# Performance work log

Hardware: AMD Instinct MI355X
Metric: run time of the kernel (lower is better)

The kernel has to match this reference:

```python
import jax, jax.numpy as jnp
import numpy as np


def _pair_table(L):
    # 0,0 0,1 ... upper-triangular (start,end) enumeration, P = L*(L+1)/2
    starts = np.concatenate([np.arange(i + 1) for i in range(L)])
    ends = np.concatenate([np.full(i + 1, i) for i in range(L)])
    return starts.astype(np.int32), ends.astype(np.int32)


def setup_inputs() -> dict:
    key = jax.random.key(0)
    ks = jax.random.split(key, 10)
    B, L, Q, H, T = 8, 384, 64, 256, 9
    p = lambda k, shape: jax.random.normal(k, shape, jnp.float32) * 0.02
    return dict(
        batch_hiddens=jax.random.normal(ks[0], (B, L, H), jnp.float32),
        batch_masks=jnp.ones((B, L), dtype=bool),
        queries=jax.random.normal(ks[1], (B, Q, H), jnp.float32),
        queries_locs=jax.random.uniform(ks[2], (B, Q, 2), jnp.float32) * L,
        queries_logits=jax.random.normal(ks[3], (B, Q, T + 1), jnp.float32),
        Wc=p(ks[4], (H, T + 1)), bc=jnp.zeros((T + 1,), jnp.float32),
        Wq=p(ks[5], (H, 2 * H)), bq=jnp.zeros((2 * H,), jnp.float32),
        Wv=p(ks[6], (H, 2 * H)), bv=jnp.zeros((2 * H,), jnp.float32),
        Wo=p(ks[7], (H, 2)), bo=jnp.zeros((2,), jnp.float32),
        Wf=p(ks[8], (H, 2)), bf=jnp.zeros((2,), jnp.float32),
    )


def reference(batch_hiddens, batch_masks, queries, queries_locs, queries_logits,
              Wc, bc, Wq, bq, Wv, bv, Wo, bo, Wf, bf):
    B, L, H = batch_hiddens.shape
    Q = queries.shape[1]
    starts, ends = _pair_table(L)  # static: L known at trace time

    # label probabilities: softmax(prior logits + classifier(queries))
    labels_pros = jax.nn.softmax(queries_logits + queries @ Wc + bc, axis=-1)

    # biaffine start/end channels
    qh = (queries @ Wq + bq).reshape(B, Q, 2, H)        # [B,Q,2,H]
    ch = (batch_hiddens @ Wv + bv).reshape(B, L, 2, H)  # [B,L,2,H]
    score = jnp.einsum('bqch,bvch->bcqv', qh, ch) / jnp.sqrt(jnp.float32(H))
    score = jnp.where(batch_masks[:, None, None, :], score, -1e8)

    # span score via start/end table gather: [B,Q,P]
    span = score[:, 0][:, :, starts] + score[:, 1][:, :, ends]
    mask_p = batch_masks[:, ends]  # [B,P] valid if end token valid

    # locator: gaussian distribution over spans centered at refined locations
    offset = queries @ Wo + bo                      # [B,Q,2]
    factors = jax.nn.softplus(queries @ Wf + bf)    # [B,Q,2] positive widths
    locs = queries_locs + offset                    # [B,Q,2]
    pairs_f = jnp.stack([jnp.asarray(starts), jnp.asarray(ends)], axis=-1).astype(jnp.float32)  # [P,2]
    d2 = (pairs_f[None, None] - locs[:, :, None]) ** 2          # [B,Q,P,2]
    weight = jnp.exp(-(d2 * factors[:, :, None]).sum(-1))       # [B,Q,P]
    weight = jnp.where(mask_p[:, None, :], weight, 0.0)

    # weighted softmax over spans
    m = jnp.max(span, axis=-1, keepdims=True)
    e = jnp.exp(span - m) * weight
    locs_pros = e / (jnp.sum(e, axis=-1, keepdims=True) + 1e-12)
    return labels_pros, locs_pros
```

## Files before the change

### kernel.cpp

```cpp
#include <hip/hip_runtime.h>
#include <math.h>

#define B_    8
#define L_    384
#define Q_    64
#define H_    256
#define R_    512
#define P_    73920
#define NF4   18480
#define QF4   4620

#define WS_WVT   0
#define WS_HIDT  131072
#define WS_G     917504
#define WS_DOTC  1179648
#define WS_LOCS  1180672
#define WS_FACT  1181696
#define WS_EXEY  1182720

__device__ __forceinline__ void tile_transpose(const float* __restrict__ in,
                                               float* __restrict__ outp,
                                               int M, int N, int mt, int nt,
                                               float* smem ) {
    float (*t)[65] = (float(*)[65])smem;
    int lane = threadIdx.x & 63, row4 = threadIdx.x >> 6;
    int m0 = mt * 64, n0 = nt * 64;
#pragma unroll
    for (int p = 0; p < 16; p++) {
        int m = m0 + p * 4 + row4;
        t[p * 4 + row4][lane] = in[m * N + n0 + lane];
    }
    __syncthreads();
#pragma unroll
    for (int p = 0; p < 16; p++) {
        int n = n0 + p * 4 + row4;
        outp[n * M + m0 + lane] = t[lane][p * 4 + row4];
    }
}

__global__ __launch_bounds__(256) void k_front(const float* __restrict__ hid,
                                               const float* __restrict__ Wv,
                                               float* __restrict__ ws) {
    __shared__ float smem[64 * 65];
    int blk = blockIdx.x;
    if (blk < 192) {
        int b = blk / 24, t = blk % 24;
        int mt = t % 6, nt = t / 6;
        tile_transpose(hid + b * 98304, ws + WS_HIDT + b * 98304, 384, 256, mt, nt, smem);
    } else {
        int t = blk - 192;
        int mt = t % 4, nt = t / 4;
        tile_transpose(Wv, ws + WS_WVT, 256, 512, mt, nt, smem);
    }
}

__global__ __launch_bounds__(512) void k_qhg(const float* __restrict__ queries,
                                             const float* __restrict__ Wq,
                                             const float* __restrict__ bq_p,
                                             const float* __restrict__ bv,
                                             const float* __restrict__ qlocs,
                                             const float* __restrict__ qlogits,
                                             const float* __restrict__ Wc,
                                             const float* __restrict__ bc,
                                             const float* __restrict__ Wo,
                                             const float* __restrict__ bo,
                                             const float* __restrict__ Wf,
                                             const float* __restrict__ bf,
                                             float* __restrict__ ws,
                                             float* __restrict__ out) {
    __shared__ float q[4][256];
    __shared__ float qh[4][512];
    int tid = threadIdx.x;
    int r0 = blockIdx.x * 4;

    for (int i = tid; i < 1024; i += 512)
        q[i >> 8][i & 255] = queries[r0 * 256 + i];
    __syncthreads();

    {
        int j = tid;
        float acc[4] = {0, 0, 0, 0};
        for (int h = 0; h < 256; h += 2) {
            float wa = Wq[h * 512 + j];
            float wb = Wq[(h + 1) * 512 + j];
#pragma unroll
            for (int r = 0; r < 4; r++)
                acc[r] += q[r][h] * wa + q[r][h + 1] * wb;
        }
        float bj = bq_p[j];
#pragma unroll
        for (int r = 0; r < 4; r++) qh[r][j] = acc[r] + bj;
    }
    __syncthreads();

    {
        int c = tid >> 8, h = tid & 255;
        const float* wvt = ws + WS_WVT + c * 65536 + h;
        float acc[4] = {0, 0, 0, 0};
        for (int hp = 0; hp < 256; hp += 2) {
            float w0 = wvt[hp * 256];
            float w1 = wvt[(hp + 1) * 256];
#pragma unroll
            for (int r = 0; r < 4; r++)
                acc[r] += qh[r][c * 256 + hp] * w0 + qh[r][c * 256 + hp + 1] * w1;
        }
#pragma unroll
        for (int r = 0; r < 4; r++)
            ws[WS_G + (r0 + r) * 512 + tid] = acc[r];
    }

    {
        int w = tid >> 6, lane = tid & 63;
        int r = w >> 1, c = w & 1;
        float v = 0.f;
#pragma unroll
        for (int k = 0; k < 4; k++) {
            int h = lane + 64 * k;
            v += qh[r][c * 256 + h] * bv[c * 256 + h];
        }
#pragma unroll
        for (int off = 32; off; off >>= 1) v += __shfl_xor(v, off);
        if (lane == 0) ws[WS_DOTC + (r0 + r) * 2 + c] = v;
    }

    {
        int w = tid >> 6, lane = tid & 63;
        if (w < 4) {
            int r = r0 + w;
            float q0 = q[w][lane];
            float q1 = q[w][lane + 64];
            float q2 = q[w][lane + 128];
            float q3 = q[w][lane + 192];

            float x[10];
#pragma unroll
            for (int t = 0; t < 10; t++) {
                float v = q0 * Wc[lane * 10 + t] + q1 * Wc[(lane + 64) * 10 + t]
                        + q2 * Wc[(lane + 128) * 10 + t] + q3 * Wc[(lane + 192) * 10 + t];
#pragma unroll
                for (int off = 32; off; off >>= 1) v += __shfl_xor(v, off);
                x[t] = qlogits[r * 10 + t] + bc[t] + v;
            }
            float m = -1e30f;
#pragma unroll
            for (int t = 0; t < 10; t++) m = fmaxf(m, x[t]);
            float s = 0.f;
#pragma unroll
            for (int t = 0; t < 10; t++) { x[t] = expf(x[t] - m); s += x[t]; }
            float inv = 1.0f / s;
            if (lane == 0) {
#pragma unroll
                for (int t = 0; t < 10; t++) out[r * 10 + t] = x[t] * inv;
            }

#pragma unroll
            for (int k = 0; k < 2; k++) {
                float vo = q0 * Wo[lane * 2 + k] + q1 * Wo[(lane + 64) * 2 + k]
                         + q2 * Wo[(lane + 128) * 2 + k] + q3 * Wo[(lane + 192) * 2 + k];
                float vf = q0 * Wf[lane * 2 + k] + q1 * Wf[(lane + 64) * 2 + k]
                         + q2 * Wf[(lane + 128) * 2 + k] + q3 * Wf[(lane + 192) * 2 + k];
#pragma unroll
                for (int off = 32; off; off >>= 1) { vo += __shfl_xor(vo, off); vf += __shfl_xor(vf, off); }
                if (lane == 0) {
                    ws[WS_LOCS + r * 2 + k] = qlocs[r * 2 + k] + vo + bo[k];
                    float xx = vf + bf[k];
                    ws[WS_FACT + r * 2 + k] = (xx > 20.f) ? xx : log1pf(expf(xx));
                }
            }
        }
    }
}

__global__ __launch_bounds__(384) void k_prep(const float* __restrict__ ws_c,
                                              float* __restrict__ ws,
                                              const int* __restrict__ mask) {
    __shared__ float g0[256], g1[256];
    __shared__ float s0[384], s1[384];
    __shared__ float Ex[384], Ey[384];
    __shared__ float scal[4];

    int tid = threadIdx.x;
    int r = blockIdx.x;
    int b = r >> 6;

    if (tid < 256) {
        g0[tid] = ws_c[WS_G + r * 512 + tid];
        g1[tid] = ws_c[WS_G + r * 512 + 256 + tid];
    }
    float dotc0 = ws_c[WS_DOTC + r * 2 + 0];
    float dotc1 = ws_c[WS_DOTC + r * 2 + 1];
    float lx = ws_c[WS_LOCS + r * 2 + 0], ly = ws_c[WS_LOCS + r * 2 + 1];
    float fx = ws_c[WS_FACT + r * 2 + 0], fy = ws_c[WS_FACT + r * 2 + 1];
    __syncthreads();

    const float* hT = ws_c + WS_HIDT + b * 98304;
    float s0r, s1r;
    bool mk;
    {
        int v = tid;
        float a0 = 0.f, a1 = 0.f;
        const float* p = hT + v;
#pragma unroll 8
        for (int h = 0; h < 256; h++) {
            float x = p[h * 384];
            a0 += x * g0[h];
            a1 += x * g1[h];
        }
        mk = mask[b * 384 + v] != 0;
        s0r = mk ? (a0 + dotc0) * 0.0625f : -1e8f;
        s1r = mk ? (a1 + dotc1) * 0.0625f : -1e8f;
        s0[v] = s0r;
        s1[v] = s1r;
    }
    __syncthreads();

    if (tid < 64) {
        int l = tid;
        float p[6];
        p[0] = s0[l * 6 + 0];
#pragma unroll
        for (int k = 1; k < 6; k++) p[k] = fmaxf(p[k - 1], s0[l * 6 + k]);
        float run = p[5];
#pragma unroll
        for (int off = 1; off < 64; off <<= 1) {
            float t = __shfl_up(run, off);
            if (l >= off) run = fmaxf(run, t);
        }
        float excl = __shfl_up(run, 1);
        if (l == 0) excl = -1e30f;
        float m0 = __shfl(run, 63);
        float lm = -1e30f, lm1 = -1e30f;
#pragma unroll
        for (int k = 0; k < 6; k++) {
            float pm = fmaxf(excl, p[k]);
            float sv = s1[l * 6 + k];
            lm = fmaxf(lm, sv + pm);
            lm1 = fmaxf(lm1, sv);
        }
#pragma unroll
        for (int off = 1; off < 64; off <<= 1) {
            lm  = fmaxf(lm,  __shfl_xor(lm,  off));
            lm1 = fmaxf(lm1, __shfl_xor(lm1, off));
        }
        if (l == 0) { scal[0] = m0; scal[1] = lm1; scal[2] = lm; }
    }
    __syncthreads();

    float m0 = scal[0], m1 = scal[1], mM = scal[2];
    float exv, eyv;
    {
        int i = tid;
        float ds = (float)i - lx;
        exv = expf(s0r - m0 - fx * ds * ds);
        float de = (float)i - ly;
        eyv = mk ? expf(s1r - m1 - fy * de * de) : 0.f;
        Ex[i] = exv;
        Ey[i] = eyv;
    }
    __syncthreads();

    if (tid < 64) {
        int l = tid;
        float p[6];
        p[0] = Ex[l * 6 + 0];
#pragma unroll
        for (int k = 1; k < 6; k++) p[k] = p[k - 1] + Ex[l * 6 + k];
        float run = p[5];
#pragma unroll
        for (int off = 1; off < 64; off <<= 1) {
            float t = __shfl_up(run, off);
            if (l >= off) run += t;
        }
        float excl = __shfl_up(run, 1);
        if (l == 0) excl = 0.f;
        float s2l = 0.f;
#pragma unroll
        for (int k = 0; k < 6; k++)
            s2l += Ey[l * 6 + k] * (excl + p[k]);
#pragma unroll
        for (int off = 1; off < 64; off <<= 1) s2l += __shfl_xor(s2l, off);
        if (l == 0) {
            float C = expf(m0 + m1 - mM);
            scal[3] = C / (C * s2l + 1e-12f);
        }
    }
    __syncthreads();

    float scale = scal[3];
    float* exr = ws + WS_EXEY + r * 768;
    exr[tid]       = exv;
    exr[384 + tid] = eyv * scale;
}

__global__ __launch_bounds__(256) void k_write(const float* __restrict__ ws,
                                               float* __restrict__ out) {
    __shared__ float exey[768];
    int tid = threadIdx.x;
    int r = blockIdx.x >> 2, q = blockIdx.x & 3;
    const float* exr = ws + WS_EXEY + r * 768;
    for (int i = tid; i < 768; i += 256) exey[i] = exr[i];
    __syncthreads();
    const float* Ex = exey;
    const float* Ey = exey + 384;

    float* ob = out + 5120 + r * 73920;
    int base = q * QF4;
    int end = base + QF4;
    for (int idx = base + tid; idx < end; idx += 256) {
        int p0 = idx << 2;
        int e = (int)((sqrtf(8.f * (float)p0 + 1.f) - 1.f) * 0.5f);
        int tri = (e * (e + 1)) >> 1;
        while (tri > p0) { e--; tri -= (e + 1); }
        while (p0 - tri > e) { tri += (e + 1); e++; }
        int s = p0 - tri;
        float ey = Ey[e];
        float4 v;
        v.x = Ex[s] * ey; if (++s > e) { s = 0; ey = Ey[++e]; }
        v.y = Ex[s] * ey; if (++s > e) { s = 0; ey = Ey[++e]; }
        v.z = Ex[s] * ey; if (++s > e) { s = 0; ey = Ey[++e]; }
        v.w = Ex[s] * ey;
        reinterpret_cast<float4*>(ob)[idx] = v;
    }
}

extern "C" void kernel_launch(void* const* d_in, const int* in_sizes, int n_in,
                              void* d_out, int out_size, void* d_ws, size_t ws_size,
                              hipStream_t stream) {
    const float* hiddens = (const float*)d_in[0];
    const int* masks     = (const int*)d_in[1];
    const float* queries = (const float*)d_in[2];
    const float* qlocs   = (const float*)d_in[3];
    const float* qlogits = (const float*)d_in[4];
    const float* Wc = (const float*)d_in[5];
    const float* bc = (const float*)d_in[6];
    const float* Wq = (const float*)d_in[7];
    const float* bq = (const float*)d_in[8];
    const float* Wv = (const float*)d_in[9];
    const float* bv = (const float*)d_in[10];
    const float* Wo = (const float*)d_in[11];
    const float* bo = (const float*)d_in[12];
    const float* Wf = (const float*)d_in[13];
    const float* bf = (const float*)d_in[14];
    float* out = (float*)d_out;
    float* ws  = (float*)d_ws;

    hipLaunchKernelGGL(k_front, dim3(224),  dim3(256), 0, stream, hiddens, Wv, ws);
    hipLaunchKernelGGL(k_qhg,   dim3(128),  dim3(512), 0, stream,
                       queries, Wq, bq, bv, qlocs, qlogits, Wc, bc, Wo, bo, Wf, bf, ws, out);
    hipLaunchKernelGGL(k_prep,  dim3(512),  dim3(384), 0, stream, ws, ws, masks);
    hipLaunchKernelGGL(k_write, dim3(2048), dim3(256), 0, stream, ws, out);
}
```

Before: 242.1 us.

## Merge transpose and query-projection kernels, drop Wv transpose, vectorize score GEMV

Fuses the hidden-state transpose and the query projection into a single launch, with block-range dispatch picking the role for each block. Wv is no longer transposed; the G computation reads Wv rows directly as float4 and dots them against qh with vectorised shared loads. In k_prep the per-token dot product over H is split into four chunks across threads, using float4 loads and a shared-memory partial reduction. This removes one launch and the Wv transpose traffic, and raises parallelism in the score GEMV, at the cost of extra shared memory and a sync.

```diff
diff --git a/kernel.cpp b/kernel.cpp
--- a/kernel.cpp
+++ b/kernel.cpp
@@ -10,71 +10,59 @@
 #define NF4   18480
 #define QF4   4620
 
-#define WS_WVT   0
-#define WS_HIDT  131072
-#define WS_G     917504
-#define WS_DOTC  1179648
-#define WS_LOCS  1180672
-#define WS_FACT  1181696
-#define WS_EXEY  1182720
-
-__device__ __forceinline__ void tile_transpose(const float* __restrict__ in,
-                                               float* __restrict__ outp,
-                                               int M, int N, int mt, int nt,
-                                               float* smem ) {
-    float (*t)[65] = (float(*)[65])smem;
-    int lane = threadIdx.x & 63, row4 = threadIdx.x >> 6;
-    int m0 = mt * 64, n0 = nt * 64;
-#pragma unroll
-    for (int p = 0; p < 16; p++) {
-        int m = m0 + p * 4 + row4;
-        t[p * 4 + row4][lane] = in[m * N + n0 + lane];
-    }
-    __syncthreads();
-#pragma unroll
-    for (int p = 0; p < 16; p++) {
-        int n = n0 + p * 4 + row4;
-        outp[n * M + m0 + lane] = t[lane][p * 4 + row4];
-    }
-}
-
-__global__ __launch_bounds__(256) void k_front(const float* __restrict__ hid,
-                                               const float* __restrict__ Wv,
-                                               float* __restrict__ ws) {
-    __shared__ float smem[64 * 65];
+#define WS_HIDT  0
+#define WS_G     786432
+#define WS_DOTC  1048576
+#define WS_LOCS  1049600
+#define WS_FACT  1050624
+#define WS_EXEY  1051648
+
+__global__ __launch_bounds__(512) void k_f1(const float* __restrict__ hid,
+                                            const float* __restrict__ Wv,
+                                            const float* __restrict__ queries,
+                                            const float* __restrict__ Wq,
+                                            const float* __restrict__ bq_p,
+                                            const float* __restrict__ bv,
+                                            const float* __restrict__ qlocs,
+                                            const float* __restrict__ qlogits,
+                                            const float* __restrict__ Wc,
+                                            const float* __restrict__ bc,
+                                            const float* __restrict__ Wo,
+                                            const float* __restrict__ bo,
+                                            const float* __restrict__ Wf,
+                                            const float* __restrict__ bf,
+                                            float* __restrict__ ws,
+                                            float* __restrict__ out) {
+    __shared__ float smem[8320];
     int blk = blockIdx.x;
-    if (blk < 192) {
-        int b = blk / 24, t = blk % 24;
-        int mt = t % 6, nt = t / 6;
-        tile_transpose(hid + b * 98304, ws + WS_HIDT + b * 98304, 384, 256, mt, nt, smem);
-    } else {
-        int t = blk - 192;
-        int mt = t % 4, nt = t / 4;
-        tile_transpose(Wv, ws + WS_WVT, 256, 512, mt, nt, smem);
-    }
-}
-
-__global__ __launch_bounds__(512) void k_qhg(const float* __restrict__ queries,
-                                             const float* __restrict__ Wq,
-                                             const float* __restrict__ bq_p,
-                                             const float* __restrict__ bv,
-                                             const float* __restrict__ qlocs,
-                                             const float* __restrict__ qlogits,
-                                             const float* __restrict__ Wc,
-                                             const float* __restrict__ bc,
-                                             const float* __restrict__ Wo,
-                                             const float* __restrict__ bo,
-                                             const float* __restrict__ Wf,
-                                             const float* __restrict__ bf,
-                                             float* __restrict__ ws,
-                                             float* __restrict__ out) {
-    __shared__ float q[4][256];
-    __shared__ float qh[4][512];
     int tid = threadIdx.x;
-    int r0 = blockIdx.x * 4;
+
+    if (blk < 96) {
+        int half = tid >> 8, lt = tid & 255;
+        int b = blk / 12;
+        int t2 = (blk % 12) * 2 + half;
+        int mt = t2 % 6, nt = t2 / 6;
+        float (*tt)[65] = (float(*)[65])(smem + half * 4160);
+        int lane = lt & 63, row4 = lt >> 6;
+        int m0 = mt * 64, n0 = nt * 64;
+        const float* in = hid + b * 98304;
+        float* op = ws + WS_HIDT + b * 98304;
+#pragma unroll
+        for (int p = 0; p < 16; p++)
+            tt[p * 4 + row4][lane] = in[(m0 + p * 4 + row4) * 256 + n0 + lane];
+        __syncthreads();
+#pragma unroll
+        for (int p = 0; p < 16; p++)
+            op[(n0 + p * 4 + row4) * 384 + m0 + lane] = tt[lane][p * 4 + row4];
+        return;
+    }
+
+    float* q  = smem;
+    float* qh = smem + 1024;
+    int r0 = (blk - 96) * 4;
 
     for (int i = tid; i < 1024; i += 512)
-        q[i >> 8][i & 255] = queries[r0 * 256 + i];
+        q[i] = queries[r0 * 256 + i];
     __syncthreads();
 
     {
@@ -85,24 +73,25 @@
             float wb = Wq[(h + 1) * 512 + j];
 #pragma unroll
             for (int r = 0; r < 4; r++)
-                acc[r] += q[r][h] * wa + q[r][h + 1] * wb;
+                acc[r] += q[r * 256 + h] * wa + q[r * 256 + h + 1] * wb;
         }
         float bj = bq_p[j];
 #pragma unroll
-        for (int r = 0; r < 4; r++) qh[r][j] = acc[r] + bj;
+        for (int r = 0; r < 4; r++) qh[r * 512 + j] = acc[r] + bj;
     }
     __syncthreads();
 
     {
         int c = tid >> 8, h = tid & 255;
-        const float* wvt = ws + WS_WVT + c * 65536 + h;
+        const float4* wv4 = (const float4*)(Wv + h * 512 + c * 256);
         float acc[4] = {0, 0, 0, 0};
-        for (int hp = 0; hp < 256; hp += 2) {
-            float w0 = wvt[hp * 256];
-            float w1 = wvt[(hp + 1) * 256];
-#pragma unroll
-            for (int r = 0; r < 4; r++)
-                acc[r] += qh[r][c * 256 + hp] * w0 + qh[r][c * 256 + hp + 1] * w1;
+        for (int hp4 = 0; hp4 < 64; hp4++) {
+            float4 w = wv4[hp4];
+#pragma unroll
+            for (int r = 0; r < 4; r++) {
+                float4 qv = *reinterpret_cast<const float4*>(&qh[r * 512 + c * 256 + hp4 * 4]);
+                acc[r] += qv.x * w.x + qv.y * w.y + qv.z * w.z + qv.w * w.w;
+            }
         }
 #pragma unroll
         for (int r = 0; r < 4; r++)
@@ -116,7 +105,7 @@
 #pragma unroll
         for (int k = 0; k < 4; k++) {
             int h = lane + 64 * k;
-            v += qh[r][c * 256 + h] * bv[c * 256 + h];
+            v += qh[r * 512 + c * 256 + h] * bv[c * 256 + h];
         }
 #pragma unroll
         for (int off = 32; off; off >>= 1) v += __shfl_xor(v, off);
@@ -127,10 +116,10 @@
         int w = tid >> 6, lane = tid & 63;
         if (w < 4) {
             int r = r0 + w;
-            float q0 = q[w][lane];
-            float q1 = q[w][lane + 64];
-            float q2 = q[w][lane + 128];
-            float q3 = q[w][lane + 192];
+            float q0 = q[w * 256 + lane];
+            float q1 = q[w * 256 + lane + 64];
+            float q2 = q[w * 256 + lane + 128];
+            float q3 = q[w * 256 + lane + 192];
 
             float x[10];
 #pragma unroll
@@ -175,6 +164,7 @@
                                               float* __restrict__ ws,
                                               const int* __restrict__ mask) {
     __shared__ float g0[256], g1[256];
+    __shared__ float part[4][96][8];
     __shared__ float s0[384], s1[384];
     __shared__ float Ex[384], Ey[384];
     __shared__ float scal[4];
@@ -194,23 +184,36 @@
     __syncthreads();
 
     const float* hT = ws_c + WS_HIDT + b * 98304;
+    {
+        int hc = tid / 96, vg = tid - hc * 96;
+        const float* pb = hT + hc * 64 * 384 + vg * 4;
+        float a0[4] = {0, 0, 0, 0}, a1[4] = {0, 0, 0, 0};
+#pragma unroll 4
+        for (int h = 0; h < 64; h++) {
+            float4 x = *reinterpret_cast<const float4*>(pb + h * 384);
+            float ga = g0[hc * 64 + h], gb = g1[hc * 64 + h];
+            a0[0] += x.x * ga; a0[1] += x.y * ga; a0[2] += x.z * ga; a0[3] += x.w * ga;
+            a1[0] += x.x * gb; a1[1] += x.y * gb; a1[2] += x.z * gb; a1[3] += x.w * gb;
+        }
+#pragma unroll
+        for (int k = 0; k < 4; k++) {
+            part[hc][vg][k]     = a0[k];
+            part[hc][vg][4 + k] = a1[k];
+        }
+    }
+    __syncthreads();
+
     float s0r, s1r;
     bool mk;
     {
-        int v = tid;
-        float a0 = 0.f, a1 = 0.f;
-        const float* p = hT + v;
-#pragma unroll 8
-        for (int h = 0; h < 256; h++) {
-            float x = p[h * 384];
-            a0 += x * g0[h];
-            a1 += x * g1[h];
-        }
-        mk = mask[b * 384 + v] != 0;
-        s0r = mk ? (a0 + dotc0) * 0.0625f : -1e8f;
-        s1r = mk ? (a1 + dotc1) * 0.0625f : -1e8f;
-        s0[v] = s0r;
-        s1[v] = s1r;
+        int vg = tid >> 2, k = tid & 3;
+        float r0 = part[0][vg][k] + part[1][vg][k] + part[2][vg][k] + part[3][vg][k];
+        float r1 = part[0][vg][4 + k] + part[1][vg][4 + k] + part[2][vg][4 + k] + part[3][vg][4 + k];
+        mk = mask[b * 384 + tid] != 0;
+        s0r = mk ? (r0 + dotc0) * 0.0625f : -1e8f;
+        s1r = mk ? (r1 + dotc1) * 0.0625f : -1e8f;
+        s0[tid] = s0r;
+        s1[tid] = s1r;
     }
     __syncthreads();
 
@@ -249,13 +252,12 @@
     float m0 = scal[0], m1 = scal[1], mM = scal[2];
     float exv, eyv;
     {
-        int i = tid;
-        float ds = (float)i - lx;
+        float ds = (float)tid - lx;
         exv = expf(s0r - m0 - fx * ds * ds);
-        float de = (float)i - ly;
+        float de = (float)tid - ly;
         eyv = mk ? expf(s1r - m1 - fy * de * de) : 0.f;
-        Ex[i] = exv;
-        Ey[i] = eyv;
+        Ex[tid] = exv;
+        Ey[tid] = eyv;
     }
     __syncthreads();
 
@@ -344,9 +346,9 @@
     float* out = (float*)d_out;
     float* ws  = (float*)d_ws;
 
-    hipLaunchKernelGGL(k_front, dim3(224),  dim3(256), 0, stream, hiddens, Wv, ws);
-    hipLaunchKernelGGL(k_qhg,   dim3(128),  dim3(512), 0, stream,
-                       queries, Wq, bq, bv, qlocs, qlogits, Wc, bc, Wo, bo, Wf, bf, ws, out);
+    hipLaunchKernelGGL(k_f1,    dim3(224),  dim3(512), 0, stream,
+                       hiddens, Wv, queries, Wq, bq, bv, qlocs, qlogits,
+                       Wc, bc, Wo, bo, Wf, bf, ws, out);
     hipLaunchKernelGGL(k_prep,  dim3(512),  dim3(384), 0, stream, ws, ws, masks);
     hipLaunchKernelGGL(k_write, dim3(2048), dim3(256), 0, stream, ws, out);
 }
```

New measurement: 244.4 us. About the same (+0.9%).
